# Performance work log

Hardware: AMD Instinct MI355X
Metric: run time of the kernel (lower is better)

Reference implementation:

```python
import jax, jax.numpy as jnp
import numpy as np

N_NODES = 200000
N_EDGES = 3200000
F_IN, HID, N_CLS = 128, 35, 10


def setup_inputs() -> dict:
    key = jax.random.key(0)
    k = jax.random.split(key, 5)
    x = jax.random.normal(k[0], (N_NODES, F_IN), dtype=jnp.float32)
    edge_index = jax.random.randint(k[1], (2, N_EDGES), 0, N_NODES, dtype=jnp.int64)
    W1 = jax.random.normal(k[2], (F_IN, HID), dtype=jnp.float32) / np.sqrt(F_IN)
    b1 = jnp.zeros((HID,), dtype=jnp.float32)
    W2 = jax.random.normal(k[3], (HID, N_CLS), dtype=jnp.float32) / np.sqrt(HID)
    b2 = jnp.zeros((N_CLS,), dtype=jnp.float32)
    return {"x": x, "edge_index": edge_index, "W1": W1, "b1": b1, "W2": W2, "b2": b2}


def _gcn_conv(x, W, b, row, col, norm, n_nodes):
    # GCNConv: linear transform, then normalized neighbor aggregation (scatter-add)
    h = x @ W                               # [N, d_out]
    msg = h[row] * norm[:, None]            # gather along edges, [E+N, d_out]
    agg = jax.ops.segment_sum(msg, col, num_segments=n_nodes)
    return agg + b


def reference(x, edge_index, W1, b1, W2, b2):
    n = x.shape[0]
    loop = jnp.arange(n, dtype=edge_index.dtype)
    row = jnp.concatenate([edge_index[0], loop])  # sources (+ self loops)
    col = jnp.concatenate([edge_index[1], loop])  # targets (+ self loops)
    deg = jax.ops.segment_sum(jnp.ones_like(col, dtype=x.dtype), col, num_segments=n)
    dinv = jnp.where(deg > 0, deg ** -0.5, 0.0)
    norm = dinv[row] * dinv[col]                  # D^{-1/2} A D^{-1/2} edge weights

    h = _gcn_conv(x, W1, b1, row, col, norm, n)
    h = jax.nn.relu(h)
    # F.dropout with training=self.training: identity at inference
    out = _gcn_conv(h, W2, b2, row, col, norm, n)
    return jax.nn.log_softmax(out, axis=1)
```

## Files before the change

kernel.cpp:

```cpp
#include <hip/hip_runtime.h>

#define NN    200000
#define F_IN  128
#define HID   35
#define LD1   36
#define LD2   12
#define NCLS  10
#define NPB   256
#define NB    782
#define CAP   5120
#define EPT   32

static __device__ inline unsigned short f2bf(float f) {
    unsigned u = __float_as_uint(f);
    u = (u + 0x7FFFu + ((u >> 16) & 1u)) >> 16;
    return (unsigned short)u;
}
static __device__ inline unsigned pk2(float a, float b) {
    return (unsigned)f2bf(a) | ((unsigned)f2bf(b) << 16);
}
static __device__ inline float bflo(unsigned u) { return __uint_as_float(u << 16); }
static __device__ inline float bfhi(unsigned u) { return __uint_as_float(u & 0xFFFF0000u); }


__global__ void k_initcur(int* __restrict__ gcur) {
    int t = threadIdx.x;
    if (t < NB) gcur[t] = t * CAP;
}

__global__ __launch_bounds__(256)
void k_bucket(const int* __restrict__ row, const int* __restrict__ col, int E,
              int* __restrict__ gcur, unsigned* __restrict__ bkt) {
    __shared__ int hist[NB];
    __shared__ int basev[NB];
    int t = threadIdx.x;
    long e0 = (long)blockIdx.x * (256 * EPT);
    for (int i = t; i < NB; i += 256) hist[i] = 0;
    __syncthreads();
    int cols[EPT];
#pragma unroll
    for (int i = 0; i < EPT; ++i) {
        long e = e0 + (long)i * 256 + t;
        if (e < E) {
            int c = col[e];
            cols[i] = c;
            atomicAdd(&hist[c >> 8], 1);
        } else cols[i] = -1;
    }
    __syncthreads();
    for (int i = t; i < NB; i += 256) {
        int h = hist[i];
        basev[i] = (h > 0) ? atomicAdd(&gcur[i], h) : 0;
        hist[i] = 0;
    }
    __syncthreads();
#pragma unroll
    for (int i = 0; i < EPT; ++i) {
        int c = cols[i];
        if (c >= 0) {
            long e = e0 + (long)i * 256 + t;
            int r = row[e];
            int b = c >> 8;
            int pos = basev[b] + atomicAdd(&hist[b], 1);
            if (pos < NB * CAP) bkt[pos] = (unsigned)r | ((unsigned)(c & 255) << 18);
        }
    }
}

__global__ __launch_bounds__(256)
void k_sort(unsigned* __restrict__ bkt, const int* __restrict__ gcur,
            int* __restrict__ obeg, int* __restrict__ oend,
            float* __restrict__ dinv, int n) {
    __shared__ unsigned est[CAP];
    __shared__ int hist[NPB];
    __shared__ int cur[NPB];
    __shared__ int sc[NPB];
    int b = blockIdx.x, t = threadIdx.x;
    int ec = gcur[b] - b * CAP;
    if (ec > CAP) ec = CAP;
    unsigned* ep = bkt + (size_t)b * CAP;
    hist[t] = 0;
    __syncthreads();
    for (int e = t; e < ec; e += 256) {
        unsigned p = ep[e];
        est[e] = p;
        atomicAdd(&hist[p >> 18], 1);
    }
    __syncthreads();
    sc[t] = hist[t];
    __syncthreads();
    for (int d = 1; d < NPB; d <<= 1) {
        int add = (t >= d) ? sc[t - d] : 0;
        __syncthreads();
        sc[t] += add;
        __syncthreads();
    }
    int excl = sc[t] - hist[t];
    cur[t] = excl;
    int i = b * NPB + t;
    if (i < n) {
        obeg[i] = b * CAP + excl;
        oend[i] = b * CAP + excl + hist[t];
        dinv[i] = rsqrtf((float)(hist[t] + 1));
    }
    __syncthreads();
    for (int e = t; e < ec; e += 256) {
        unsigned p = est[e];
        int lc = p >> 18;
        int pos = atomicAdd(&cur[lc], 1);
        ep[pos] = p & 0x3FFFF;
    }
}


__global__ void k_gemm1(const float* __restrict__ x, const float* __restrict__ W1,
                        const float* __restrict__ dinv,
                        unsigned short* __restrict__ hs1A,
                        unsigned short* __restrict__ hs1B, int n) {
    int i = blockIdx.x * blockDim.x + threadIdx.x;
    if (i >= n) return;
    float acc[HID];
#pragma unroll
    for (int j = 0; j < HID; ++j) acc[j] = 0.f;
    const float4* xr = (const float4*)(x + (size_t)i * F_IN);
    for (int k4 = 0; k4 < F_IN / 4; ++k4) {
        float4 xv = xr[k4];
        const float* w = W1 + (size_t)(k4 * 4) * HID;
#pragma unroll
        for (int j = 0; j < HID; ++j)
            acc[j] += xv.x * w[j] + xv.y * w[HID + j] + xv.z * w[2 * HID + j] + xv.w * w[3 * HID + j];
    }
    float d = dinv[i];
    unsigned* oa = (unsigned*)(hs1A + (size_t)i * 32);
#pragma unroll
    for (int j = 0; j < 16; ++j) oa[j] = pk2(acc[2 * j] * d, acc[2 * j + 1] * d);
    unsigned* ob = (unsigned*)(hs1B + (size_t)i * 4);
    ob[0] = pk2(acc[32] * d, acc[33] * d);
    ob[1] = pk2(acc[34] * d, 0.f);
}

__global__ void k_agg1(const int* __restrict__ obeg, const int* __restrict__ oend,
                       const unsigned* __restrict__ srow,
                       const unsigned short* __restrict__ A,
                       const unsigned short* __restrict__ Bf,
                       float* __restrict__ acc1, int n) {
    int wid = (blockIdx.x * blockDim.x + threadIdx.x) >> 6;
    int lane = threadIdx.x & 63;
    if (wid >= n) return;
    int s = lane & 15;
    int g = lane >> 4;
    int beg = obeg[wid], end = oend[wid];
    float a0=0.f,a1=0.f,a2=0.f,a3=0.f,a4=0.f,a5=0.f,a6=0.f,a7=0.f;
    float b0=0.f,b1=0.f,b2=0.f;
    int e = beg + s;
    unsigned idx = (e < end) ? srow[e] : 0xFFFFFFFFu;
    for (int base = beg; base < end; base += 16) {
        int en = base + 16 + s;
        unsigned nidx = (en < end) ? srow[en] : 0xFFFFFFFFu;
        bool v = (idx != 0xFFFFFFFFu);
        unsigned r = v ? idx : (unsigned)wid;
        uint4 av = *(const uint4*)(A + ((size_t)r << 5) + (g << 3));
        if (v) {
            a0 += bflo(av.x); a1 += bfhi(av.x);
            a2 += bflo(av.y); a3 += bfhi(av.y);
            a4 += bflo(av.z); a5 += bfhi(av.z);
            a6 += bflo(av.w); a7 += bfhi(av.w);
        }
        if (lane < 16 && v) {
            uint2 bv = *(const uint2*)(Bf + ((size_t)r << 2));
            b0 += bflo(bv.x); b1 += bfhi(bv.x); b2 += bflo(bv.y);
        }
        idx = nidx;
    }
#pragma unroll
    for (int d = 1; d < 16; d <<= 1) {
        a0 += __shfl_xor(a0, d); a1 += __shfl_xor(a1, d);
        a2 += __shfl_xor(a2, d); a3 += __shfl_xor(a3, d);
        a4 += __shfl_xor(a4, d); a5 += __shfl_xor(a5, d);
        a6 += __shfl_xor(a6, d); a7 += __shfl_xor(a7, d);
        b0 += __shfl_xor(b0, d); b1 += __shfl_xor(b1, d); b2 += __shfl_xor(b2, d);
    }
    if (s == 0) {
        uint4 sv = *(const uint4*)(A + ((size_t)wid << 5) + (g << 3));
        a0 += bflo(sv.x); a1 += bfhi(sv.x);
        a2 += bflo(sv.y); a3 += bfhi(sv.y);
        a4 += bflo(sv.z); a5 += bfhi(sv.z);
        a6 += bflo(sv.w); a7 += bfhi(sv.w);
        float* o = acc1 + (size_t)wid * LD1 + (g << 3);
        *(float4*)o       = make_float4(a0, a1, a2, a3);
        *(float4*)(o + 4) = make_float4(a4, a5, a6, a7);
    }
    if (lane == 0) {
        uint2 sb = *(const uint2*)(Bf + ((size_t)wid << 2));
        b0 += bflo(sb.x); b1 += bfhi(sb.x); b2 += bflo(sb.y);
        *(float4*)(acc1 + (size_t)wid * LD1 + 32) = make_float4(b0, b1, b2, 0.f);
    }
}


__global__ void k_layer2(const float* __restrict__ acc1, const float* __restrict__ dinv,
                         const float* __restrict__ b1, const float* __restrict__ W2,
                         unsigned short* __restrict__ hs2b, int n) {
    int i = blockIdx.x * blockDim.x + threadIdx.x;
    if (i >= n) return;
    float d = dinv[i];
    const float4* a = (const float4*)(acc1 + (size_t)i * LD1);
    float4 tq[9];
#pragma unroll
    for (int q = 0; q < 9; ++q) tq[q] = a[q];
    const float* tf = (const float*)tq;
    float h[HID];
#pragma unroll
    for (int k = 0; k < HID; ++k) {
        float v = tf[k] * d + b1[k];
        h[k] = v > 0.f ? v : 0.f;
    }
    float o[NCLS];
#pragma unroll
    for (int j = 0; j < NCLS; ++j) o[j] = 0.f;
#pragma unroll
    for (int k = 0; k < HID; ++k) {
#pragma unroll
        for (int j = 0; j < NCLS; ++j) o[j] += h[k] * W2[k * NCLS + j];
    }
    unsigned* dst = (unsigned*)(hs2b + (size_t)i * LD2);
#pragma unroll
    for (int j = 0; j < 5; ++j) dst[j] = pk2(o[2 * j] * d, o[2 * j + 1] * d);
    dst[5] = 0u;
}

__global__ void k_agg2o(const int* __restrict__ obeg, const int* __restrict__ oend,
                        const unsigned* __restrict__ srow,
                        const unsigned short* __restrict__ H,
                        const float* __restrict__ dinv, const float* __restrict__ b2,
                        float* __restrict__ out, int n) {
    int wid = (blockIdx.x * blockDim.x + threadIdx.x) >> 6;
    int lane = threadIdx.x & 63;
    if (wid >= n) return;
    int s = lane & 15;
    int g = lane >> 4;
    int beg = obeg[wid], end = oend[wid];
    float a0=0.f,a1=0.f,a2=0.f,a3=0.f;
    int e = beg + s;
    unsigned idx = (e < end) ? srow[e] : 0xFFFFFFFFu;
    for (int base = beg; base < end; base += 16) {
        int en = base + 16 + s;
        unsigned nidx = (en < end) ? srow[en] : 0xFFFFFFFFu;
        bool v = (idx != 0xFFFFFFFFu);
        unsigned r = v ? idx : (unsigned)wid;
        uint2 hv = make_uint2(0u, 0u);
        if (g < 3) hv = *(const uint2*)(H + (size_t)r * LD2 + (g << 2));
        if (v) {
            a0 += bflo(hv.x); a1 += bfhi(hv.x);
            a2 += bflo(hv.y); a3 += bfhi(hv.y);
        }
        idx = nidx;
    }
#pragma unroll
    for (int d = 1; d < 16; d <<= 1) {
        a0 += __shfl_xor(a0, d); a1 += __shfl_xor(a1, d);
        a2 += __shfl_xor(a2, d); a3 += __shfl_xor(a3, d);
    }
    float v0 = -1e30f, v1 = -1e30f, v2 = -1e30f, v3 = -1e30f;
    float dn = dinv[wid];
    if (s == 0 && g < 3) {
        uint2 sv = *(const uint2*)(H + (size_t)wid * LD2 + (g << 2));
        a0 += bflo(sv.x); a1 += bfhi(sv.x);
        a2 += bflo(sv.y); a3 += bfhi(sv.y);
        int f0 = g << 2;
        v0 = a0 * dn + b2[f0];
        v1 = a1 * dn + b2[f0 + 1];
        if (f0 + 2 < NCLS) {
            v2 = a2 * dn + b2[f0 + 2];
            v3 = a3 * dn + b2[f0 + 3];
        }
    }
    float m = fmaxf(fmaxf(v0, v1), fmaxf(v2, v3));
    m = fmaxf(m, __shfl_xor(m, 16));
    m = fmaxf(m, __shfl_xor(m, 32));
    float e0 = (v0 > -1e29f) ? expf(v0 - m) : 0.f;
    float e1 = (v1 > -1e29f) ? expf(v1 - m) : 0.f;
    float e2 = (v2 > -1e29f) ? expf(v2 - m) : 0.f;
    float e3 = (v3 > -1e29f) ? expf(v3 - m) : 0.f;
    float sm = (e0 + e1) + (e2 + e3);
    sm += __shfl_xor(sm, 16);
    sm += __shfl_xor(sm, 32);
    if (s == 0 && g < 3) {
        float l = logf(sm);
        int f0 = g << 2;
        float* o = out + (size_t)wid * NCLS + f0;
        *(float2*)o = make_float2(v0 - m - l, v1 - m - l);
        if (f0 + 2 < NCLS) *(float2*)(o + 2) = make_float2(v2 - m - l, v3 - m - l);
    }
}

extern "C" void kernel_launch(void* const* d_in, const int* in_sizes, int n_in,
                              void* d_out, int out_size, void* d_ws, size_t ws_size,
                              hipStream_t stream) {
    const float* x  = (const float*)d_in[0];
    const int*   ei = (const int*)d_in[1];
    const float* W1 = (const float*)d_in[2];
    const float* b1 = (const float*)d_in[3];
    const float* W2 = (const float*)d_in[4];
    const float* b2 = (const float*)d_in[5];
    float* out = (float*)d_out;

    const int n = in_sizes[0] / F_IN;
    const int E = in_sizes[1] / 2;
    const int* row = ei;
    const int* col = ei + E;

    unsigned*       bkt  = (unsigned*)d_ws;
    int*            gcur = (int*)d_ws + 4003840;
    int*            obeg = (int*)d_ws + 4004864;
    int*            oend = (int*)d_ws + 4204864;
    float*          dinv = (float*)d_ws + 4404864;
    unsigned short* hs1A = (unsigned short*)((unsigned*)d_ws + 4604864);
    unsigned short* hs1B = (unsigned short*)((unsigned*)d_ws + 7804864);
    float*          acc1 = (float*)d_ws + 8204864;
    unsigned short* hs2b = hs1A;

    const int B = 256;
    const int nbk = (E + B * EPT - 1) / (B * EPT);

    k_initcur<<<1, 1024, 0, stream>>>(gcur);
    k_bucket<<<nbk, B, 0, stream>>>(row, col, E, gcur, bkt);
    k_sort<<<NB, B, 0, stream>>>(bkt, gcur, obeg, oend, dinv, n);

    k_gemm1<<<(n + B - 1) / B, B, 0, stream>>>(x, W1, dinv, hs1A, hs1B, n);
    k_agg1<<<(n * 64 + B - 1) / B, B, 0, stream>>>(obeg, oend, bkt, hs1A, hs1B, acc1, n);
    k_layer2<<<(n + B - 1) / B, B, 0, stream>>>(acc1, dinv, b1, W2, hs2b, n);
    k_agg2o<<<(n * 64 + B - 1) / B, B, 0, stream>>>(obeg, oend, bkt, hs2b, dinv, b2, out, n);
}
```

Before: 325.4 us.

## Process two destination nodes per wavefront in both aggregation kernels

Both gather-aggregation kernels now assign two destination nodes to each 64-lane wavefront and interleave their edge loops, so two independent gathers are in flight per iteration. This halves the number of wavefronts launched and is meant to raise memory-level parallelism and amortise per-wave setup and reduction cost. The layer-2 hidden buffer row stride is also padded from 12 to 16 bf16 so row addresses become shift-based and 32-byte aligned. In exchange the register count roughly doubles, the software prefetch of the next index is dropped, and the loop runs to the longer of the two nodes' edge lists.

```diff
diff --git a/kernel.cpp b/kernel.cpp
--- a/kernel.cpp
+++ b/kernel.cpp
@@ -5,11 +5,13 @@
 #define HID   35
 #define LD1   36
 #define LD2   12
+#define LD2P  16
 #define NCLS  10
 #define NPB   256
 #define NB    782
 #define CAP   5120
 #define EPT   32
+#define NOE   0xFFFFFFFFu
 
 static __device__ inline unsigned short f2bf(float f) {
     unsigned u = __float_as_uint(f);
@@ -144,56 +146,93 @@
                        const unsigned short* __restrict__ A,
                        const unsigned short* __restrict__ Bf,
                        float* __restrict__ acc1, int n) {
-    int wid = (blockIdx.x * blockDim.x + threadIdx.x) >> 6;
+    int wv = (blockIdx.x * blockDim.x + threadIdx.x) >> 6;
     int lane = threadIdx.x & 63;
-    if (wid >= n) return;
+    int w0 = wv * 2, w1 = w0 + 1;
+    if (w0 >= n) return;
+    bool has1 = (w1 < n);
     int s = lane & 15;
     int g = lane >> 4;
-    int beg = obeg[wid], end = oend[wid];
-    float a0=0.f,a1=0.f,a2=0.f,a3=0.f,a4=0.f,a5=0.f,a6=0.f,a7=0.f;
-    float b0=0.f,b1=0.f,b2=0.f;
-    int e = beg + s;
-    unsigned idx = (e < end) ? srow[e] : 0xFFFFFFFFu;
-    for (int base = beg; base < end; base += 16) {
-        int en = base + 16 + s;
-        unsigned nidx = (en < end) ? srow[en] : 0xFFFFFFFFu;
-        bool v = (idx != 0xFFFFFFFFu);
-        unsigned r = v ? idx : (unsigned)wid;
-        uint4 av = *(const uint4*)(A + ((size_t)r << 5) + (g << 3));
-        if (v) {
-            a0 += bflo(av.x); a1 += bfhi(av.x);
-            a2 += bflo(av.y); a3 += bfhi(av.y);
-            a4 += bflo(av.z); a5 += bfhi(av.z);
-            a6 += bflo(av.w); a7 += bfhi(av.w);
-        }
-        if (lane < 16 && v) {
-            uint2 bv = *(const uint2*)(Bf + ((size_t)r << 2));
-            b0 += bflo(bv.x); b1 += bfhi(bv.x); b2 += bflo(bv.y);
-        }
-        idx = nidx;
+    bool bl = (lane < 16);
+    int beg0 = obeg[w0], end0 = oend[w0];
+    int beg1 = has1 ? obeg[w1] : 0, end1 = has1 ? oend[w1] : 0;
+    int nb0 = end0 - beg0, nb1 = end1 - beg1;
+    int iters = max((nb0 + 15) >> 4, (nb1 + 15) >> 4);
+    float p0a=0.f,p0b=0.f,p0c=0.f,p0d=0.f,p0e=0.f,p0f=0.f,p0g=0.f,p0h=0.f;
+    float p1a=0.f,p1b=0.f,p1c=0.f,p1d=0.f,p1e=0.f,p1f=0.f,p1g=0.f,p1h=0.f;
+    float q0a=0.f,q0b=0.f,q0c=0.f, q1a=0.f,q1b=0.f,q1c=0.f;
+    int e0 = beg0 + s, e1 = beg1 + s;
+    for (int it = 0; it < iters; ++it) {
+        unsigned idx0 = (e0 < end0) ? srow[e0] : NOE;
+        unsigned idx1 = (has1 && e1 < end1) ? srow[e1] : NOE;
+        bool v0 = (idx0 != NOE), v1 = (idx1 != NOE);
+        unsigned r0 = v0 ? idx0 : (unsigned)w0;
+        unsigned r1 = v1 ? idx1 : (unsigned)w0;
+        uint4 av0 = *(const uint4*)(A + ((size_t)r0 << 5) + (g << 3));
+        uint4 av1 = *(const uint4*)(A + ((size_t)r1 << 5) + (g << 3));
+        uint2 bv0 = make_uint2(0u, 0u), bv1 = make_uint2(0u, 0u);
+        if (bl) {
+            bv0 = *(const uint2*)(Bf + ((size_t)r0 << 2));
+            bv1 = *(const uint2*)(Bf + ((size_t)r1 << 2));
+        }
+        if (v0) {
+            p0a += bflo(av0.x); p0b += bfhi(av0.x);
+            p0c += bflo(av0.y); p0d += bfhi(av0.y);
+            p0e += bflo(av0.z); p0f += bfhi(av0.z);
+            p0g += bflo(av0.w); p0h += bfhi(av0.w);
+            if (bl) { q0a += bflo(bv0.x); q0b += bfhi(bv0.x); q0c += bflo(bv0.y); }
+        }
+        if (v1) {
+            p1a += bflo(av1.x); p1b += bfhi(av1.x);
+            p1c += bflo(av1.y); p1d += bfhi(av1.y);
+            p1e += bflo(av1.z); p1f += bfhi(av1.z);
+            p1g += bflo(av1.w); p1h += bfhi(av1.w);
+            if (bl) { q1a += bflo(bv1.x); q1b += bfhi(bv1.x); q1c += bflo(bv1.y); }
+        }
+        e0 += 16; e1 += 16;
     }
 #pragma unroll
     for (int d = 1; d < 16; d <<= 1) {
-        a0 += __shfl_xor(a0, d); a1 += __shfl_xor(a1, d);
-        a2 += __shfl_xor(a2, d); a3 += __shfl_xor(a3, d);
-        a4 += __shfl_xor(a4, d); a5 += __shfl_xor(a5, d);
-        a6 += __shfl_xor(a6, d); a7 += __shfl_xor(a7, d);
-        b0 += __shfl_xor(b0, d); b1 += __shfl_xor(b1, d); b2 += __shfl_xor(b2, d);
+        p0a += __shfl_xor(p0a, d); p0b += __shfl_xor(p0b, d);
+        p0c += __shfl_xor(p0c, d); p0d += __shfl_xor(p0d, d);
+        p0e += __shfl_xor(p0e, d); p0f += __shfl_xor(p0f, d);
+        p0g += __shfl_xor(p0g, d); p0h += __shfl_xor(p0h, d);
+        p1a += __shfl_xor(p1a, d); p1b += __shfl_xor(p1b, d);
+        p1c += __shfl_xor(p1c, d); p1d += __shfl_xor(p1d, d);
+        p1e += __shfl_xor(p1e, d); p1f += __shfl_xor(p1f, d);
+        p1g += __shfl_xor(p1g, d); p1h += __shfl_xor(p1h, d);
+        q0a += __shfl_xor(q0a, d); q0b += __shfl_xor(q0b, d); q0c += __shfl_xor(q0c, d);
+        q1a += __shfl_xor(q1a, d); q1b += __shfl_xor(q1b, d); q1c += __shfl_xor(q1c, d);
     }
     if (s == 0) {
-        uint4 sv = *(const uint4*)(A + ((size_t)wid << 5) + (g << 3));
-        a0 += bflo(sv.x); a1 += bfhi(sv.x);
-        a2 += bflo(sv.y); a3 += bfhi(sv.y);
-        a4 += bflo(sv.z); a5 += bfhi(sv.z);
-        a6 += bflo(sv.w); a7 += bfhi(sv.w);
-        float* o = acc1 + (size_t)wid * LD1 + (g << 3);
-        *(float4*)o       = make_float4(a0, a1, a2, a3);
-        *(float4*)(o + 4) = make_float4(a4, a5, a6, a7);
+        uint4 sv0 = *(const uint4*)(A + ((size_t)w0 << 5) + (g << 3));
+        p0a += bflo(sv0.x); p0b += bfhi(sv0.x);
+        p0c += bflo(sv0.y); p0d += bfhi(sv0.y);
+        p0e += bflo(sv0.z); p0f += bfhi(sv0.z);
+        p0g += bflo(sv0.w); p0h += bfhi(sv0.w);
+        float* o0 = acc1 + (size_t)w0 * LD1 + (g << 3);
+        *(float4*)o0       = make_float4(p0a, p0b, p0c, p0d);
+        *(float4*)(o0 + 4) = make_float4(p0e, p0f, p0g, p0h);
+        if (has1) {
+            uint4 sv1 = *(const uint4*)(A + ((size_t)w1 << 5) + (g << 3));
+            p1a += bflo(sv1.x); p1b += bfhi(sv1.x);
+            p1c += bflo(sv1.y); p1d += bfhi(sv1.y);
+            p1e += bflo(sv1.z); p1f += bfhi(sv1.z);
+            p1g += bflo(sv1.w); p1h += bfhi(sv1.w);
+            float* o1 = acc1 + (size_t)w1 * LD1 + (g << 3);
+            *(float4*)o1       = make_float4(p1a, p1b, p1c, p1d);
+            *(float4*)(o1 + 4) = make_float4(p1e, p1f, p1g, p1h);
+        }
     }
     if (lane == 0) {
-        uint2 sb = *(const uint2*)(Bf + ((size_t)wid << 2));
-        b0 += bflo(sb.x); b1 += bfhi(sb.x); b2 += bflo(sb.y);
-        *(float4*)(acc1 + (size_t)wid * LD1 + 32) = make_float4(b0, b1, b2, 0.f);
+        uint2 sb0 = *(const uint2*)(Bf + ((size_t)w0 << 2));
+        q0a += bflo(sb0.x); q0b += bfhi(sb0.x); q0c += bflo(sb0.y);
+        *(float4*)(acc1 + (size_t)w0 * LD1 + 32) = make_float4(q0a, q0b, q0c, 0.f);
+        if (has1) {
+            uint2 sb1 = *(const uint2*)(Bf + ((size_t)w1 << 2));
+            q1a += bflo(sb1.x); q1b += bfhi(sb1.x); q1c += bflo(sb1.y);
+            *(float4*)(acc1 + (size_t)w1 * LD1 + 32) = make_float4(q1a, q1b, q1c, 0.f);
+        }
     }
 }
 
@@ -223,10 +262,10 @@
 #pragma unroll
         for (int j = 0; j < NCLS; ++j) o[j] += h[k] * W2[k * NCLS + j];
     }
-    unsigned* dst = (unsigned*)(hs2b + (size_t)i * LD2);
+    unsigned* dst = (unsigned*)(hs2b + (size_t)i * LD2P);
 #pragma unroll
     for (int j = 0; j < 5; ++j) dst[j] = pk2(o[2 * j] * d, o[2 * j + 1] * d);
-    dst[5] = 0u;
+    dst[5] = 0u; dst[6] = 0u; dst[7] = 0u;
 }
 
 __global__ void k_agg2o(const int* __restrict__ obeg, const int* __restrict__ oend,
@@ -234,63 +273,91 @@
                         const unsigned short* __restrict__ H,
                         const float* __restrict__ dinv, const float* __restrict__ b2,
                         float* __restrict__ out, int n) {
-    int wid = (blockIdx.x * blockDim.x + threadIdx.x) >> 6;
+    int wv = (blockIdx.x * blockDim.x + threadIdx.x) >> 6;
     int lane = threadIdx.x & 63;
-    if (wid >= n) return;
+    int w0 = wv * 2, w1 = w0 + 1;
+    if (w0 >= n) return;
+    bool has1 = (w1 < n);
     int s = lane & 15;
     int g = lane >> 4;
-    int beg = obeg[wid], end = oend[wid];
+    bool ga = (g < 3);
+    int beg0 = obeg[w0], end0 = oend[w0];
+    int beg1 = has1 ? obeg[w1] : 0, end1 = has1 ? oend[w1] : 0;
+    int nb0 = end0 - beg0, nb1 = end1 - beg1;
+    int iters = max((nb0 + 15) >> 4, (nb1 + 15) >> 4);
     float a0=0.f,a1=0.f,a2=0.f,a3=0.f;
-    int e = beg + s;
-    unsigned idx = (e < end) ? srow[e] : 0xFFFFFFFFu;
-    for (int base = beg; base < end; base += 16) {
-        int en = base + 16 + s;
-        unsigned nidx = (en < end) ? srow[en] : 0xFFFFFFFFu;
-        bool v = (idx != 0xFFFFFFFFu);
-        unsigned r = v ? idx : (unsigned)wid;
-        uint2 hv = make_uint2(0u, 0u);
-        if (g < 3) hv = *(const uint2*)(H + (size_t)r * LD2 + (g << 2));
-        if (v) {
-            a0 += bflo(hv.x); a1 += bfhi(hv.x);
-            a2 += bflo(hv.y); a3 += bfhi(hv.y);
-        }
-        idx = nidx;
+    float c0=0.f,c1=0.f,c2=0.f,c3=0.f;
+    int e0 = beg0 + s, e1 = beg1 + s;
+    for (int it = 0; it < iters; ++it) {
+        unsigned idx0 = (e0 < end0) ? srow[e0] : NOE;
+        unsigned idx1 = (has1 && e1 < end1) ? srow[e1] : NOE;
+        bool v0 = (idx0 != NOE), v1 = (idx1 != NOE);
+        unsigned r0 = v0 ? idx0 : (unsigned)w0;
+        unsigned r1 = v1 ? idx1 : (unsigned)w0;
+        uint2 h0 = make_uint2(0u,0u), h1 = make_uint2(0u,0u);
+        if (ga) {
+            h0 = *(const uint2*)(H + ((size_t)r0 << 4) + (g << 2));
+            h1 = *(const uint2*)(H + ((size_t)r1 << 4) + (g << 2));
+        }
+        if (v0) { a0 += bflo(h0.x); a1 += bfhi(h0.x); a2 += bflo(h0.y); a3 += bfhi(h0.y); }
+        if (v1) { c0 += bflo(h1.x); c1 += bfhi(h1.x); c2 += bflo(h1.y); c3 += bfhi(h1.y); }
+        e0 += 16; e1 += 16;
     }
 #pragma unroll
     for (int d = 1; d < 16; d <<= 1) {
         a0 += __shfl_xor(a0, d); a1 += __shfl_xor(a1, d);
         a2 += __shfl_xor(a2, d); a3 += __shfl_xor(a3, d);
-    }
-    float v0 = -1e30f, v1 = -1e30f, v2 = -1e30f, v3 = -1e30f;
-    float dn = dinv[wid];
-    if (s == 0 && g < 3) {
-        uint2 sv = *(const uint2*)(H + (size_t)wid * LD2 + (g << 2));
-        a0 += bflo(sv.x); a1 += bfhi(sv.x);
-        a2 += bflo(sv.y); a3 += bfhi(sv.y);
+        c0 += __shfl_xor(c0, d); c1 += __shfl_xor(c1, d);
+        c2 += __shfl_xor(c2, d); c3 += __shfl_xor(c3, d);
+    }
+    float v0_=-1e30f, v1_=-1e30f, v2_=-1e30f, v3_=-1e30f;
+    if (s == 0 && ga) {
+        uint2 sv = *(const uint2*)(H + ((size_t)w0 << 4) + (g << 2));
+        a0 += bflo(sv.x); a1 += bfhi(sv.x); a2 += bflo(sv.y); a3 += bfhi(sv.y);
+        float dn = dinv[w0];
         int f0 = g << 2;
-        v0 = a0 * dn + b2[f0];
-        v1 = a1 * dn + b2[f0 + 1];
-        if (f0 + 2 < NCLS) {
-            v2 = a2 * dn + b2[f0 + 2];
-            v3 = a3 * dn + b2[f0 + 3];
-        }
-    }
-    float m = fmaxf(fmaxf(v0, v1), fmaxf(v2, v3));
+        v0_ = a0 * dn + b2[f0];
+        v1_ = a1 * dn + b2[f0 + 1];
+        if (f0 + 2 < NCLS) { v2_ = a2 * dn + b2[f0 + 2]; v3_ = a3 * dn + b2[f0 + 3]; }
+    }
+    float m = fmaxf(fmaxf(v0_, v1_), fmaxf(v2_, v3_));
     m = fmaxf(m, __shfl_xor(m, 16));
     m = fmaxf(m, __shfl_xor(m, 32));
-    float e0 = (v0 > -1e29f) ? expf(v0 - m) : 0.f;
-    float e1 = (v1 > -1e29f) ? expf(v1 - m) : 0.f;
-    float e2 = (v2 > -1e29f) ? expf(v2 - m) : 0.f;
-    float e3 = (v3 > -1e29f) ? expf(v3 - m) : 0.f;
-    float sm = (e0 + e1) + (e2 + e3);
-    sm += __shfl_xor(sm, 16);
-    sm += __shfl_xor(sm, 32);
-    if (s == 0 && g < 3) {
-        float l = logf(sm);
+    float s0 = ((v0_ > -1e29f) ? expf(v0_ - m) : 0.f) + ((v1_ > -1e29f) ? expf(v1_ - m) : 0.f)
+             + ((v2_ > -1e29f) ? expf(v2_ - m) : 0.f) + ((v3_ > -1e29f) ? expf(v3_ - m) : 0.f);
+    s0 += __shfl_xor(s0, 16);
+    s0 += __shfl_xor(s0, 32);
+    if (s == 0 && ga) {
+        float l = logf(s0);
         int f0 = g << 2;
-        float* o = out + (size_t)wid * NCLS + f0;
-        *(float2*)o = make_float2(v0 - m - l, v1 - m - l);
-        if (f0 + 2 < NCLS) *(float2*)(o + 2) = make_float2(v2 - m - l, v3 - m - l);
+        float* o = out + (size_t)w0 * NCLS + f0;
+        *(float2*)o = make_float2(v0_ - m - l, v1_ - m - l);
+        if (f0 + 2 < NCLS) *(float2*)(o + 2) = make_float2(v2_ - m - l, v3_ - m - l);
+    }
+    if (!has1) return;
+    float u0=-1e30f, u1=-1e30f, u2=-1e30f, u3=-1e30f;
+    if (s == 0 && ga) {
+        uint2 sv = *(const uint2*)(H + ((size_t)w1 << 4) + (g << 2));
+        c0 += bflo(sv.x); c1 += bfhi(sv.x); c2 += bflo(sv.y); c3 += bfhi(sv.y);
+        float dn = dinv[w1];
+        int f0 = g << 2;
+        u0 = c0 * dn + b2[f0];
+        u1 = c1 * dn + b2[f0 + 1];
+        if (f0 + 2 < NCLS) { u2 = c2 * dn + b2[f0 + 2]; u3 = c3 * dn + b2[f0 + 3]; }
+    }
+    float m1 = fmaxf(fmaxf(u0, u1), fmaxf(u2, u3));
+    m1 = fmaxf(m1, __shfl_xor(m1, 16));
+    m1 = fmaxf(m1, __shfl_xor(m1, 32));
+    float s1 = ((u0 > -1e29f) ? expf(u0 - m1) : 0.f) + ((u1 > -1e29f) ? expf(u1 - m1) : 0.f)
+             + ((u2 > -1e29f) ? expf(u2 - m1) : 0.f) + ((u3 > -1e29f) ? expf(u3 - m1) : 0.f);
+    s1 += __shfl_xor(s1, 16);
+    s1 += __shfl_xor(s1, 32);
+    if (s == 0 && ga) {
+        float l = logf(s1);
+        int f0 = g << 2;
+        float* o = out + (size_t)w1 * NCLS + f0;
+        *(float2*)o = make_float2(u0 - m1 - l, u1 - m1 - l);
+        if (f0 + 2 < NCLS) *(float2*)(o + 2) = make_float2(u2 - m1 - l, u3 - m1 - l);
     }
 }
 
@@ -322,13 +389,14 @@
 
     const int B = 256;
     const int nbk = (E + B * EPT - 1) / (B * EPT);
+    const int npair = (n + 1) / 2;
 
     k_initcur<<<1, 1024, 0, stream>>>(gcur);
     k_bucket<<<nbk, B, 0, stream>>>(row, col, E, gcur, bkt);
     k_sort<<<NB, B, 0, stream>>>(bkt, gcur, obeg, oend, dinv, n);
 
     k_gemm1<<<(n + B - 1) / B, B, 0, stream>>>(x, W1, dinv, hs1A, hs1B, n);
-    k_agg1<<<(n * 64 + B - 1) / B, B, 0, stream>>>(obeg, oend, bkt, hs1A, hs1B, acc1, n);
+    k_agg1<<<(npair * 64 + B - 1) / B, B, 0, stream>>>(obeg, oend, bkt, hs1A, hs1B, acc1, n);
     k_layer2<<<(n + B - 1) / B, B, 0, stream>>>(acc1, dinv, b1, W2, hs2b, n);
-    k_agg2o<<<(n * 64 + B - 1) / B, B, 0, stream>>>(obeg, oend, bkt, hs2b, dinv, b2, out, n);
-}
+    k_agg2o<<<(npair * 64 + B - 1) / B, B, 0, stream>>>(obeg, oend, bkt, hs2b, dinv, b2, out, n);
+}
```

After: 307.1 us. 5.6% less time.
